# Kernel optimization log

Measured on AMD Instinct MI355X. Metric: run time of the kernel, lower is better.

The kernel has to match this reference:

```python
import jax, jax.numpy as jnp
import numpy as np

C = 128   # desc_dim
NQ = 8
NK = 32768

def setup_inputs() -> dict:
    k = jax.random.key(0)
    ks = jax.random.split(k, 9)
    query = jax.random.normal(ks[0], (1, C, NQ), dtype=jnp.float32)
    keys = jax.random.normal(ks[1], (1, C, NK), dtype=jnp.float32)
    value = jax.random.normal(ks[2], (1, C, NK), dtype=jnp.float32)
    dist = jax.random.normal(ks[3], (1, C, NQ * NK), dtype=jnp.float32)
    mask = jax.random.randint(ks[4], (1, NQ, NK), 0, 2).astype(bool)
    # MLP([3C, C, 1]) as 1x1 Conv1d weights (kernel size 1 -> plain matmuls)
    W1 = jax.random.normal(ks[5], (C, 3 * C), dtype=jnp.float32) * (1.0 / np.sqrt(3 * C))
    b1 = jax.random.normal(ks[6], (C,), dtype=jnp.float32) * 0.01
    W2 = jax.random.normal(ks[7], (1, C), dtype=jnp.float32) * (1.0 / np.sqrt(C))
    b2 = jax.random.normal(ks[8], (1,), dtype=jnp.float32) * 0.01
    return {"query": query, "keys": keys, "value": value, "dist": dist,
            "mask": mask, "W1": W1, "b1": b1, "W2": W2, "b2": b2}

def reference(query, keys, value, dist, mask, W1, b1, W2, b2):
    b = query.shape[0]
    nq, nk = query.shape[-1], keys.shape[-1]
    # pairwise concat: [b, 3C, nq*nk] (faithful to the torch repeat-expand)
    q_e = jnp.broadcast_to(query[:, :, :, None], (b, query.shape[1], nq, nk)).reshape(b, -1, nq * nk)
    k_e = jnp.broadcast_to(keys[:, :, None, :], (b, keys.shape[1], nq, nk)).reshape(b, -1, nq * nk)
    cat = jnp.concatenate([q_e, k_e, dist], axis=1)            # [b, 3C, nq*nk]
    h = jax.nn.relu(jnp.einsum('oc,bcl->bol', W1, cat) + b1[None, :, None])
    s = jnp.einsum('oc,bcl->bol', W2, h) + b2[None, :, None]   # [b, 1, nq*nk]
    scores = s.reshape(b, nq, nk)
    # mask branch (bool tensor): push masked-out entries below the min
    floor = jax.lax.stop_gradient(scores.min()) - 20.0
    scores = scores + floor * (~mask).astype(scores.dtype).reshape(1, nq, nk)
    prob = jax.nn.softmax(scores, axis=-1)                     # [b, nq, nk]
    out = jnp.einsum('bnm,bdm->bdn', prob, value)              # [b, C, nq]
    return out, scores
```

## Files before the change

kernel.cpp:

```cpp
#include <hip/hip_runtime.h>
#include <hip/hip_bf16.h>
#include <math.h>

#define C_    128
#define NQ_   8
#define NK_   32768
#define QNK_  (NQ_*NK_)
#define KW_   16
#define KTB_  64
#define NSB_  512
#define NCH_  256

#define AQ_OFF     0
#define MINKEY_OFF 1024
#define DENOM_OFF  1040
#define OUTV_OFF   4096
#define WSA_OFF    266240

typedef float f32x4 __attribute__((ext_vector_type(4)));
typedef int   i32x4 __attribute__((ext_vector_type(4)));
typedef short bf16x8 __attribute__((ext_vector_type(8)));

__device__ inline unsigned short f2bf(float f){
  unsigned u = __float_as_uint(f);
  return (unsigned short)((u + 0x7FFFu + ((u >> 16) & 1u)) >> 16);
}
__device__ inline unsigned int pkbf(float a, float b){
  __hip_bfloat162 h = __float22bfloat162_rn(make_float2(a, b));
  union { __hip_bfloat162 h2; unsigned int u; } cv; cv.h2 = h; return cv.u;
}
__device__ inline unsigned int fkey(float f){
  unsigned u = __float_as_uint(f);
  return (u & 0x80000000u) ? ~u : (u | 0x80000000u);
}
__device__ inline float fkey_dec(unsigned key){
  unsigned u = (key & 0x80000000u) ? (key & 0x7FFFFFFFu) : ~key;
  return __uint_as_float(u);
}
__device__ inline int swz8(int r){ return ((r ^ (r >> 3)) & 7) << 3; }

__global__ __launch_bounds__(256) void prep_kernel(const float* __restrict__ query,
    const float* __restrict__ W1, const float* __restrict__ b1, float* __restrict__ ws){
  const int t = threadIdx.x, b = blockIdx.x;
  if (b < 16){
    unsigned int* wsa = (unsigned int*)(ws + WSA_OFF);
    for (int u = b*1024 + t; u < (b+1)*1024; u += 256){
      unsigned int pack = 0;
#pragma unroll
      for (int e2 = 0; e2 < 2; e2++){
        const int E = u*2 + e2;
        const int f = E >> 9, lane = (E >> 3) & 63, e = E & 7;
        const int w = f >> 4, r = f & 15;
        const int part = r >> 3, ks = (r >> 1) & 3, of = r & 1;
        const int o = w*32 + of*16 + (lane & 15);
        const int c = ks*32 + ((lane >> 4) << 3) + e;
        pack |= (unsigned int)f2bf(W1[o*384 + 128 + part*128 + c]) << (16*e2);
      }
      wsa[u] = pack;
    }
  } else {
    if (t == 0) *(unsigned int*)(ws + MINKEY_OFF) = 0xFFFFFFFFu;
    if (t < 128){
      const int o = t;
      float s[8];
#pragma unroll
      for (int q = 0; q < 8; q++) s[q] = b1[o];
      for (int c = 0; c < 128; c++){
        const float wv = W1[o*384 + c];
#pragma unroll
        for (int q = 0; q < 8; q++) s[q] += wv * query[c*8 + q];
      }
#pragma unroll
      for (int q = 0; q < 8; q++) ws[AQ_OFF + q*128 + o] = s[q];
    }
  }
}

__device__ inline void stage16_load(const float* __restrict__ src, size_t rstride,
                                    int l, f32x4* ra, f32x4* rb){
  const int skl = (l & 3) * 4;
  const int c2  = (l >> 2) * 2;
#pragma unroll
  for (int p = 0; p < 4; p++){
    const float* pa = src + (size_t)(p*32 + c2)*rstride + skl;
    ra[p] = __builtin_nontemporal_load((const f32x4*)pa);
    rb[p] = __builtin_nontemporal_load((const f32x4*)(pa + rstride));
  }
}
__device__ inline void stage16_write(unsigned short* __restrict__ lds,
                                     int l, const f32x4* ra, const f32x4* rb){
  const int skl = (l & 3) * 4;
  const int c2  = (l >> 2) * 2;
#pragma unroll
  for (int p = 0; p < 4; p++){
    const int c = p*32 + c2;
#pragma unroll
    for (int j = 0; j < 4; j++){
      const int kl = skl + j;
      const int idx = (kl*128 + c) ^ swz8(kl);
      *(unsigned int*)&lds[idx] = pkbf(ra[p][j], rb[p][j]);
    }
  }
}
__device__ inline bf16x8 frag16_read(const unsigned short* __restrict__ lds,
                                     int ks, int g, int li){
  const int idx = (li << 7) + (((ks << 5) + (g << 3)) ^ swz8(li));
  return *(const bf16x8*)&lds[idx];
}

__global__ __launch_bounds__(256, 2) void scores_kernel(
    const float* __restrict__ keys, const float* __restrict__ dist,
    const float* __restrict__ W2, const float* __restrict__ b2p,
    float* __restrict__ ws, float* __restrict__ scores)
{
  __shared__ unsigned short a_lds[32*512];
  __shared__ unsigned short d_lds[4][KW_*128];
  __shared__ float aq_lds[NQ_*128];
  __shared__ float w2_lds[128];
  __shared__ float minred[4];

  const int t = threadIdx.x, w = t >> 6, l = t & 63;
  const int g = l >> 4, li = l & 15;
  const int blk = blockIdx.x;
  const int k0w = blk*KTB_ + w*KW_;
  unsigned short* dw = d_lds[w];

  const unsigned int* wsaU = (const unsigned int*)(ws + WSA_OFF);
  unsigned int* aU = (unsigned int*)a_lds;
  for (int i = t; i < 8192; i += 256){
    const int s = i >> 8, r = i & 255;
    aU[i] = wsaU[((s >> 3)*16 + (s & 7))*256 + r];
  }
  for (int i = t; i < NQ_*128; i += 256) aq_lds[i] = ws[AQ_OFF + i];
  if (t < 128) w2_lds[t] = W2[t];

  f32x4 rA[4], rB[4], rC[4], rD[4];
  stage16_load(keys + k0w, NK_, l, rA, rB);
  stage16_write(dw, l, rA, rB);
  stage16_load(dist + k0w, QNK_, l, rA, rB);
  __syncthreads();

  f32x4 bk[8];
#pragma unroll
  for (int f = 0; f < 8; f++){ f32x4 z = {0.f,0.f,0.f,0.f}; bk[f] = z; }
#pragma unroll
  for (int ks = 0; ks < 4; ks++){
    const bf16x8 bfr = frag16_read(dw, ks, g, li);
#pragma unroll
    for (int of8 = 0; of8 < 8; of8++){
      const int s = (of8 >> 1)*8 + ks*2 + (of8 & 1);
      const bf16x8 a = *(const bf16x8*)&a_lds[s*512 + l*8];
      bk[of8] = __builtin_amdgcn_mfma_f32_16x16x32_bf16(a, bfr, bk[of8], 0,0,0);
    }
  }
  __syncthreads();

  for (int i = t; i < 8192; i += 256){
    const int s = i >> 8, r = i & 255;
    aU[i] = wsaU[((s >> 3)*16 + 8 + (s & 7))*256 + r];
  }
  __syncthreads();

  const float b2v = b2p[0];
  float minv = INFINITY;

#define SCORE_ITER(Q, RA, RB, RA2, RB2)                                          \
  {                                                                              \
    if ((Q) < 7) stage16_load(dist + (size_t)((Q)+1)*NK_ + k0w, QNK_, l, RA2, RB2); \
    stage16_write(dw, l, RA, RB);                                                \
    f32x4 acc[8];                                                                \
    _Pragma("unroll")                                                            \
    for (int f = 0; f < 8; f++) acc[f] = bk[f];                                  \
    _Pragma("unroll")                                                            \
    for (int ks = 0; ks < 4; ks++){                                              \
      const bf16x8 bfr = frag16_read(dw, ks, g, li);                             \
      _Pragma("unroll")                                                          \
      for (int of8 = 0; of8 < 8; of8++){                                         \
        const int s = (of8 >> 1)*8 + ks*2 + (of8 & 1);                           \
        const bf16x8 a = *(const bf16x8*)&a_lds[s*512 + l*8];                    \
        acc[of8] = __builtin_amdgcn_mfma_f32_16x16x32_bf16(a, bfr, acc[of8], 0,0,0); \
      }                                                                          \
    }                                                                            \
    float sv = 0.f;                                                              \
    _Pragma("unroll")                                                            \
    for (int of8 = 0; of8 < 8; of8++){                                           \
      const int ob = (of8 >> 1)*32 + (of8 & 1)*16 + g*4;                         \
      const f32x4 aqv = *(const f32x4*)&aq_lds[(Q)*128 + ob];                    \
      const f32x4 w2v = *(const f32x4*)&w2_lds[ob];                              \
      _Pragma("unroll")                                                          \
      for (int r = 0; r < 4; r++)                                                \
        sv += w2v[r] * fmaxf(acc[of8][r] + aqv[r], 0.f);                         \
    }                                                                            \
    sv += __shfl_xor(sv, 16, 64);                                                \
    sv += __shfl_xor(sv, 32, 64);                                                \
    sv += b2v;                                                                   \
    if (l < 16)                                                                  \
      __builtin_nontemporal_store(sv, &scores[(size_t)(Q)*NK_ + k0w + l]);       \
    minv = fminf(minv, sv);                                                      \
  }

  SCORE_ITER(0, rA, rB, rC, rD)
  SCORE_ITER(1, rC, rD, rA, rB)
  SCORE_ITER(2, rA, rB, rC, rD)
  SCORE_ITER(3, rC, rD, rA, rB)
  SCORE_ITER(4, rA, rB, rC, rD)
  SCORE_ITER(5, rC, rD, rA, rB)
  SCORE_ITER(6, rA, rB, rC, rD)
  SCORE_ITER(7, rC, rD, rA, rB)
#undef SCORE_ITER

#pragma unroll
  for (int off = 32; off > 0; off >>= 1) minv = fminf(minv, __shfl_xor(minv, off, 64));
  if (l == 0) minred[w] = minv;
  __syncthreads();
  if (t == 0){
    const float m = fminf(fminf(minred[0], minred[1]), fminf(minred[2], minred[3]));
    atomicMin((unsigned int*)(ws + MINKEY_OFF), fkey(m));
  }
}

__global__ __launch_bounds__(256) void softmax_pv_kernel(
    const float* __restrict__ value, const int* __restrict__ mask,
    float* __restrict__ scores, float* __restrict__ ws)
{
  __shared__ float v_lds[128*128];
  __shared__ __align__(16) float e_lds[8][128];
  __shared__ float wsum[8];
  const int t = threadIdx.x, bid = blockIdx.x, k0 = bid*128;
  const float floorv = fkey_dec(*(const unsigned int*)(ws + MINKEY_OFF)) - 20.0f;

  for (int i = t; i < 4096; i += 256){
    const int d = i >> 5, k4 = (i & 31)*4;
    const f32x4 v = __builtin_nontemporal_load((const f32x4*)&value[(size_t)d*NK_ + k0 + k4]);
    const int dw = (d*128 + k4) ^ ((d & 31) << 2);
    *(f32x4*)&v_lds[dw] = v;
  }

  {
    const int q = t >> 5, kk = (t & 31)*4;
    const size_t gi = (size_t)q*NK_ + k0 + kk;
    const f32x4 s4 = *(const f32x4*)&scores[gi];
    const i32x4 m4 = *(const i32x4*)&mask[gi];
    f32x4 sf, e;
#pragma unroll
    for (int j = 0; j < 4; j++){
      sf[j] = m4[j] ? s4[j] : s4[j] + floorv;
      e[j]  = __expf(sf[j]);
    }
    __builtin_nontemporal_store(sf, (f32x4*)&scores[gi]);
    *(f32x4*)&e_lds[q][kk] = e;
    float es = e[0] + e[1] + e[2] + e[3];
#pragma unroll
    for (int off = 16; off > 0; off >>= 1) es += __shfl_xor(es, off, 64);
    if ((t & 31) == 0) wsum[q] = es;
  }
  __syncthreads();
  if (t < 8) ws[DENOM_OFF + t*NCH_ + bid] = wsum[t];

  const int d = t & 127, qb = (t >> 7)*4;
  f32x4 acc = {0.f,0.f,0.f,0.f};
#pragma unroll 8
  for (int k4 = 0; k4 < 128; k4 += 4){
    const int dw = (d*128 + k4) ^ ((d & 31) << 2);
    const f32x4 v  = *(const f32x4*)&v_lds[dw];
    const f32x4 e0 = *(const f32x4*)&e_lds[qb+0][k4];
    const f32x4 e1 = *(const f32x4*)&e_lds[qb+1][k4];
    const f32x4 e2 = *(const f32x4*)&e_lds[qb+2][k4];
    const f32x4 e3 = *(const f32x4*)&e_lds[qb+3][k4];
#pragma unroll
    for (int j = 0; j < 4; j++){
      acc[0] += v[j]*e0[j]; acc[1] += v[j]*e1[j];
      acc[2] += v[j]*e2[j]; acc[3] += v[j]*e3[j];
    }
  }
#pragma unroll
  for (int j = 0; j < 4; j++) ws[OUTV_OFF + (size_t)bid*1024 + d*8 + qb + j] = acc[j];
}

__global__ __launch_bounds__(256) void finalize_kernel(const float* __restrict__ ws,
    float* __restrict__ out){
  __shared__ float dsum[8];
  __shared__ float red[8][32];
  const int t = threadIdx.x, bid = blockIdx.x;

  if (t < 64){
    const int q = t >> 3, i = t & 7;
    float s = 0.f;
    for (int j = 0; j < 32; j++) s += ws[DENOM_OFF + q*NCH_ + i + 8*j];
#pragma unroll
    for (int off = 4; off > 0; off >>= 1) s += __shfl_xor(s, off, 64);
    if (i == 0) dsum[q] = s;
  }

  const int ol = t & 31, part = t >> 5;
  float s = 0.f;
  for (int j = 0; j < 32; j++)
    s += ws[OUTV_OFF + (size_t)(part + 8*j)*1024 + bid*32 + ol];
  red[part][ol] = s;
  __syncthreads();

  if (t < 32){
    float a = 0.f;
#pragma unroll
    for (int p = 0; p < 8; p++) a += red[p][t];
    const int o = bid*32 + t;
    out[o] = a / dsum[o & 7];
  }
}

extern "C" void kernel_launch(void* const* d_in, const int* in_sizes, int n_in,
                              void* d_out, int out_size, void* d_ws, size_t ws_size,
                              hipStream_t stream){
  const float* query=(const float*)d_in[0];
  const float* keys =(const float*)d_in[1];
  const float* value=(const float*)d_in[2];
  const float* dist =(const float*)d_in[3];
  const int*   mask =(const int*)d_in[4];
  const float* W1   =(const float*)d_in[5];
  const float* b1   =(const float*)d_in[6];
  const float* W2   =(const float*)d_in[7];
  const float* b2   =(const float*)d_in[8];
  float* out=(float*)d_out;
  float* scores=out+1024;
  float* ws=(float*)d_ws;

  prep_kernel      <<<17,256,0,stream>>>(query,W1,b1,ws);
  scores_kernel    <<<NSB_,256,0,stream>>>(keys,dist,W2,b2,ws,scores);
  softmax_pv_kernel<<<NCH_,256,0,stream>>>(value,mask,scores,ws);
  finalize_kernel  <<<32,256,0,stream>>>(ws,out);
}
```

Before: 65.69 us.

## Split scores blocks across query halves with 512-thread blocks and 128-key tiles

The scores kernel now uses 512-thread blocks covering 128 keys. Each of the 512 blocks handles one half of the query dimension, so a block runs 4 query iterations per wave instead of 8. This shortens each wave's serial chain and raises the number of resident waves, at the cost of computing the key-projection MFMA twice (once per query half) and loading the weight tile into LDS for each half. The prep kernel also splits the per-query dot product across two threads and combines them with a shuffle.

```diff
diff --git a/kernel.cpp b/kernel.cpp
--- a/kernel.cpp
+++ b/kernel.cpp
@@ -7,7 +7,7 @@
 #define NK_   32768
 #define QNK_  (NQ_*NK_)
 #define KW_   16
-#define KTB_  64
+#define KTB_  128
 #define NSB_  512
 #define NCH_  256
 
@@ -60,18 +60,19 @@
     }
   } else {
     if (t == 0) *(unsigned int*)(ws + MINKEY_OFF) = 0xFFFFFFFFu;
-    if (t < 128){
-      const int o = t;
-      float s[8];
-#pragma unroll
-      for (int q = 0; q < 8; q++) s[q] = b1[o];
-      for (int c = 0; c < 128; c++){
-        const float wv = W1[o*384 + c];
-#pragma unroll
-        for (int q = 0; q < 8; q++) s[q] += wv * query[c*8 + q];
-      }
-#pragma unroll
-      for (int q = 0; q < 8; q++) ws[AQ_OFF + q*128 + o] = s[q];
+    const int o = t >> 1, h = t & 1;
+    float s[8];
+#pragma unroll
+    for (int q = 0; q < 8; q++) s[q] = 0.f;
+    for (int c = h*64; c < h*64 + 64; c++){
+      const float wv = W1[o*384 + c];
+#pragma unroll
+      for (int q = 0; q < 8; q++) s[q] += wv * query[c*8 + q];
+    }
+#pragma unroll
+    for (int q = 0; q < 8; q++){
+      s[q] += __shfl_xor(s[q], 1, 64);
+      if (h == 0) ws[AQ_OFF + q*128 + o] = s[q] + b1[o];
     }
   }
 }
@@ -108,36 +109,37 @@
   return *(const bf16x8*)&lds[idx];
 }
 
-__global__ __launch_bounds__(256, 2) void scores_kernel(
+__global__ __launch_bounds__(512, 4) void scores_kernel(
     const float* __restrict__ keys, const float* __restrict__ dist,
     const float* __restrict__ W2, const float* __restrict__ b2p,
     float* __restrict__ ws, float* __restrict__ scores)
 {
   __shared__ unsigned short a_lds[32*512];
-  __shared__ unsigned short d_lds[4][KW_*128];
-  __shared__ float aq_lds[NQ_*128];
+  __shared__ unsigned short d_lds[8][KW_*128];
+  __shared__ float aq_lds[4*128];
   __shared__ float w2_lds[128];
-  __shared__ float minred[4];
+  __shared__ float minred[8];
 
   const int t = threadIdx.x, w = t >> 6, l = t & 63;
   const int g = l >> 4, li = l & 15;
-  const int blk = blockIdx.x;
-  const int k0w = blk*KTB_ + w*KW_;
+  const int kb = blockIdx.x >> 1, qh = blockIdx.x & 1;
+  const int q0 = qh*4;
+  const int k0w = kb*KTB_ + w*KW_;
   unsigned short* dw = d_lds[w];
 
   const unsigned int* wsaU = (const unsigned int*)(ws + WSA_OFF);
   unsigned int* aU = (unsigned int*)a_lds;
-  for (int i = t; i < 8192; i += 256){
+  for (int i = t; i < 8192; i += 512){
     const int s = i >> 8, r = i & 255;
     aU[i] = wsaU[((s >> 3)*16 + (s & 7))*256 + r];
   }
-  for (int i = t; i < NQ_*128; i += 256) aq_lds[i] = ws[AQ_OFF + i];
+  aq_lds[t & 511] = ws[AQ_OFF + q0*128 + (t & 511)];
   if (t < 128) w2_lds[t] = W2[t];
 
-  f32x4 rA[4], rB[4], rC[4], rD[4];
-  stage16_load(keys + k0w, NK_, l, rA, rB);
-  stage16_write(dw, l, rA, rB);
-  stage16_load(dist + k0w, QNK_, l, rA, rB);
+  f32x4 rA[4], rB[4], kA[4], kB[4];
+  stage16_load(keys + k0w, NK_, l, kA, kB);
+  stage16_load(dist + (size_t)q0*NK_ + k0w, QNK_, l, rA, rB);
+  stage16_write(dw, l, kA, kB);
   __syncthreads();
 
   f32x4 bk[8];
@@ -155,7 +157,7 @@
   }
   __syncthreads();
 
-  for (int i = t; i < 8192; i += 256){
+  for (int i = t; i < 8192; i += 512){
     const int s = i >> 8, r = i & 255;
     aU[i] = wsaU[((s >> 3)*16 + 8 + (s & 7))*256 + r];
   }
@@ -164,57 +166,51 @@
   const float b2v = b2p[0];
   float minv = INFINITY;
 
-#define SCORE_ITER(Q, RA, RB, RA2, RB2)                                          \
-  {                                                                              \
-    if ((Q) < 7) stage16_load(dist + (size_t)((Q)+1)*NK_ + k0w, QNK_, l, RA2, RB2); \
-    stage16_write(dw, l, RA, RB);                                                \
-    f32x4 acc[8];                                                                \
-    _Pragma("unroll")                                                            \
-    for (int f = 0; f < 8; f++) acc[f] = bk[f];                                  \
-    _Pragma("unroll")                                                            \
-    for (int ks = 0; ks < 4; ks++){                                              \
-      const bf16x8 bfr = frag16_read(dw, ks, g, li);                             \
-      _Pragma("unroll")                                                          \
-      for (int of8 = 0; of8 < 8; of8++){                                         \
-        const int s = (of8 >> 1)*8 + ks*2 + (of8 & 1);                           \
-        const bf16x8 a = *(const bf16x8*)&a_lds[s*512 + l*8];                    \
-        acc[of8] = __builtin_amdgcn_mfma_f32_16x16x32_bf16(a, bfr, acc[of8], 0,0,0); \
-      }                                                                          \
-    }                                                                            \
-    float sv = 0.f;                                                              \
-    _Pragma("unroll")                                                            \
-    for (int of8 = 0; of8 < 8; of8++){                                           \
-      const int ob = (of8 >> 1)*32 + (of8 & 1)*16 + g*4;                         \
-      const f32x4 aqv = *(const f32x4*)&aq_lds[(Q)*128 + ob];                    \
-      const f32x4 w2v = *(const f32x4*)&w2_lds[ob];                              \
-      _Pragma("unroll")                                                          \
-      for (int r = 0; r < 4; r++)                                                \
-        sv += w2v[r] * fmaxf(acc[of8][r] + aqv[r], 0.f);                         \
-    }                                                                            \
-    sv += __shfl_xor(sv, 16, 64);                                                \
-    sv += __shfl_xor(sv, 32, 64);                                                \
-    sv += b2v;                                                                   \
-    if (l < 16)                                                                  \
-      __builtin_nontemporal_store(sv, &scores[(size_t)(Q)*NK_ + k0w + l]);       \
-    minv = fminf(minv, sv);                                                      \
-  }
-
-  SCORE_ITER(0, rA, rB, rC, rD)
-  SCORE_ITER(1, rC, rD, rA, rB)
-  SCORE_ITER(2, rA, rB, rC, rD)
-  SCORE_ITER(3, rC, rD, rA, rB)
-  SCORE_ITER(4, rA, rB, rC, rD)
-  SCORE_ITER(5, rC, rD, rA, rB)
-  SCORE_ITER(6, rA, rB, rC, rD)
-  SCORE_ITER(7, rC, rD, rA, rB)
-#undef SCORE_ITER
+#pragma unroll
+  for (int qi = 0; qi < 4; qi++){
+    stage16_write(dw, l, rA, rB);
+    if (qi < 3) stage16_load(dist + (size_t)(q0+qi+1)*NK_ + k0w, QNK_, l, rA, rB);
+
+    f32x4 acc[8];
+#pragma unroll
+    for (int f = 0; f < 8; f++) acc[f] = bk[f];
+#pragma unroll
+    for (int ks = 0; ks < 4; ks++){
+      const bf16x8 bfr = frag16_read(dw, ks, g, li);
+#pragma unroll
+      for (int of8 = 0; of8 < 8; of8++){
+        const int s = (of8 >> 1)*8 + ks*2 + (of8 & 1);
+        const bf16x8 a = *(const bf16x8*)&a_lds[s*512 + l*8];
+        acc[of8] = __builtin_amdgcn_mfma_f32_16x16x32_bf16(a, bfr, acc[of8], 0,0,0);
+      }
+    }
+
+    float sv = 0.f;
+#pragma unroll
+    for (int of8 = 0; of8 < 8; of8++){
+      const int ob = (of8 >> 1)*32 + (of8 & 1)*16 + g*4;
+      const f32x4 aqv = *(const f32x4*)&aq_lds[qi*128 + ob];
+      const f32x4 w2v = *(const f32x4*)&w2_lds[ob];
+#pragma unroll
+      for (int r = 0; r < 4; r++)
+        sv += w2v[r] * fmaxf(acc[of8][r] + aqv[r], 0.f);
+    }
+    sv += __shfl_xor(sv, 16, 64);
+    sv += __shfl_xor(sv, 32, 64);
+    sv += b2v;
+    if (l < 16)
+      __builtin_nontemporal_store(sv, &scores[(size_t)(q0+qi)*NK_ + k0w + l]);
+    minv = fminf(minv, sv);
+  }
 
 #pragma unroll
   for (int off = 32; off > 0; off >>= 1) minv = fminf(minv, __shfl_xor(minv, off, 64));
   if (l == 0) minred[w] = minv;
   __syncthreads();
   if (t == 0){
-    const float m = fminf(fminf(minred[0], minred[1]), fminf(minred[2], minred[3]));
+    float m = minred[0];
+#pragma unroll
+    for (int i = 1; i < 8; i++) m = fminf(m, minred[i]);
     atomicMin((unsigned int*)(ws + MINKEY_OFF), fkey(m));
   }
 }
@@ -325,7 +321,7 @@
   float* ws=(float*)d_ws;
 
   prep_kernel      <<<17,256,0,stream>>>(query,W1,b1,ws);
-  scores_kernel    <<<NSB_,256,0,stream>>>(keys,dist,W2,b2,ws,scores);
+  scores_kernel    <<<NSB_,512,0,stream>>>(keys,dist,W2,b2,ws,scores);
   softmax_pv_kernel<<<NCH_,256,0,stream>>>(value,mask,scores,ws);
   finalize_kernel  <<<32,256,0,stream>>>(ws,out);
 }
```

Measured after the change: 85.22 us. +29.7%, slower.

## Split key projection into separate kernel and halve query work per scores block

Applied to the files above, without the earlier changes.

The per-key W1_k·keys product moves into a new bkprep kernel that stores it as bf16 in the workspace. The scores kernel then launches twice as many blocks, each covering half the queries and reading that precomputed term, with occupancy raised to 3 blocks per CU. The query-bias prep is also split across thread pairs. This aims to expose more parallelism and drop the in-kernel key GEMM and the A-fragment reload. The cost is an extra launch, workspace round-trips, and bf16 rounding of the key term.

```diff
diff --git a/kernel.cpp b/kernel.cpp
--- a/kernel.cpp
+++ b/kernel.cpp
@@ -6,9 +6,6 @@
 #define NQ_   8
 #define NK_   32768
 #define QNK_  (NQ_*NK_)
-#define KW_   16
-#define KTB_  64
-#define NSB_  512
 #define NCH_  256
 
 #define AQ_OFF     0
@@ -16,10 +13,12 @@
 #define DENOM_OFF  1040
 #define OUTV_OFF   4096
 #define WSA_OFF    266240
+#define BH_OFF     282624
 
 typedef float f32x4 __attribute__((ext_vector_type(4)));
 typedef int   i32x4 __attribute__((ext_vector_type(4)));
 typedef short bf16x8 __attribute__((ext_vector_type(8)));
+typedef unsigned int u32x2 __attribute__((ext_vector_type(2)));
 
 __device__ inline unsigned short f2bf(float f){
   unsigned u = __float_as_uint(f);
@@ -29,6 +28,8 @@
   __hip_bfloat162 h = __float22bfloat162_rn(make_float2(a, b));
   union { __hip_bfloat162 h2; unsigned int u; } cv; cv.h2 = h; return cv.u;
 }
+__device__ inline float bf_lo(unsigned u){ return __uint_as_float(u << 16); }
+__device__ inline float bf_hi(unsigned u){ return __uint_as_float(u & 0xFFFF0000u); }
 __device__ inline unsigned int fkey(float f){
   unsigned u = __float_as_uint(f);
   return (u & 0x80000000u) ? ~u : (u | 0x80000000u);
@@ -60,22 +61,24 @@
     }
   } else {
     if (t == 0) *(unsigned int*)(ws + MINKEY_OFF) = 0xFFFFFFFFu;
-    if (t < 128){
-      const int o = t;
-      float s[8];
-#pragma unroll
-      for (int q = 0; q < 8; q++) s[q] = b1[o];
-      for (int c = 0; c < 128; c++){
-        const float wv = W1[o*384 + c];
-#pragma unroll
-        for (int q = 0; q < 8; q++) s[q] += wv * query[c*8 + q];
-      }
-#pragma unroll
-      for (int q = 0; q < 8; q++) ws[AQ_OFF + q*128 + o] = s[q];
-    }
-  }
-}
-
+    const int o = t >> 1, h = t & 1;
+    float s[8];
+#pragma unroll
+    for (int q = 0; q < 8; q++) s[q] = 0.f;
+    for (int c = h*64; c < h*64 + 64; c++){
+      const float wv = W1[o*384 + c];
+#pragma unroll
+      for (int q = 0; q < 8; q++) s[q] += wv * query[c*8 + q];
+    }
+#pragma unroll
+    for (int q = 0; q < 8; q++){
+      s[q] += __shfl_xor(s[q], 1, 64);
+      if (h == 0) ws[AQ_OFF + q*128 + o] = s[q] + b1[o];
+    }
+  }
+}
+
+template<bool NT>
 __device__ inline void stage16_load(const float* __restrict__ src, size_t rstride,
                                     int l, f32x4* ra, f32x4* rb){
   const int skl = (l & 3) * 4;
@@ -83,8 +86,9 @@
 #pragma unroll
   for (int p = 0; p < 4; p++){
     const float* pa = src + (size_t)(p*32 + c2)*rstride + skl;
-    ra[p] = __builtin_nontemporal_load((const f32x4*)pa);
-    rb[p] = __builtin_nontemporal_load((const f32x4*)(pa + rstride));
+    if (NT){ ra[p] = __builtin_nontemporal_load((const f32x4*)pa);
+             rb[p] = __builtin_nontemporal_load((const f32x4*)(pa + rstride)); }
+    else   { ra[p] = *(const f32x4*)pa; rb[p] = *(const f32x4*)(pa + rstride); }
   }
 }
 __device__ inline void stage16_write(unsigned short* __restrict__ lds,
@@ -108,69 +112,99 @@
   return *(const bf16x8*)&lds[idx];
 }
 
-__global__ __launch_bounds__(256, 2) void scores_kernel(
-    const float* __restrict__ keys, const float* __restrict__ dist,
-    const float* __restrict__ W2, const float* __restrict__ b2p,
-    float* __restrict__ ws, float* __restrict__ scores)
+__global__ __launch_bounds__(256) void bkprep_kernel(const float* __restrict__ keys,
+    float* __restrict__ ws){
+  __shared__ unsigned short d_lds[4][16*128];
+  const int t = threadIdx.x, w = t >> 6, l = t & 63;
+  const int g = l >> 4, li = l & 15;
+  const int kw = blockIdx.x*4 + w;
+  const int k0w = kw*16;
+  unsigned short* dw = d_lds[w];
+
+  const bf16x8* wsa8 = (const bf16x8*)(ws + WSA_OFF);
+  bf16x8 afk[32];
+#pragma unroll
+  for (int s = 0; s < 32; s++) afk[s] = wsa8[((s >> 3)*16 + (s & 7))*64 + l];
+
+  f32x4 ra[4], rb[4];
+  stage16_load<false>(keys + k0w, NK_, l, ra, rb);
+  stage16_write(dw, l, ra, rb);
+
+  f32x4 bk[8];
+#pragma unroll
+  for (int f = 0; f < 8; f++){ f32x4 z = {0.f,0.f,0.f,0.f}; bk[f] = z; }
+#pragma unroll
+  for (int ks = 0; ks < 4; ks++){
+    const bf16x8 bfr = frag16_read(dw, ks, g, li);
+#pragma unroll
+    for (int of8 = 0; of8 < 8; of8++){
+      const int s = (of8 >> 1)*8 + ks*2 + (of8 & 1);
+      bk[of8] = __builtin_amdgcn_mfma_f32_16x16x32_bf16(afk[s], bfr, bk[of8], 0,0,0);
+    }
+  }
+
+  unsigned int* bh = (unsigned int*)(ws + BH_OFF);
+#pragma unroll
+  for (int of8 = 0; of8 < 8; of8++){
+    u32x2 p;
+    p[0] = pkbf(bk[of8][0], bk[of8][1]);
+    p[1] = pkbf(bk[of8][2], bk[of8][3]);
+    *(u32x2*)(bh + (size_t)((kw*8 + of8)*64 + l)*2) = p;
+  }
+}
+
+__global__ __launch_bounds__(256, 3) void scores_kernel(
+    const float* __restrict__ dist, const float* __restrict__ W2,
+    const float* __restrict__ b2p, float* __restrict__ ws,
+    float* __restrict__ scores)
 {
   __shared__ unsigned short a_lds[32*512];
-  __shared__ unsigned short d_lds[4][KW_*128];
-  __shared__ float aq_lds[NQ_*128];
+  __shared__ unsigned short d_lds[4][16*128];
+  __shared__ float aq_lds[4*128];
   __shared__ float w2_lds[128];
   __shared__ float minred[4];
 
   const int t = threadIdx.x, w = t >> 6, l = t & 63;
   const int g = l >> 4, li = l & 15;
-  const int blk = blockIdx.x;
-  const int k0w = blk*KTB_ + w*KW_;
+  const int kb = blockIdx.x >> 1, qh = blockIdx.x & 1;
+  const int q0 = qh*4;
+  const int kw = kb*4 + w;
+  const int k0w = kw*16;
   unsigned short* dw = d_lds[w];
 
   const unsigned int* wsaU = (const unsigned int*)(ws + WSA_OFF);
   unsigned int* aU = (unsigned int*)a_lds;
   for (int i = t; i < 8192; i += 256){
     const int s = i >> 8, r = i & 255;
-    aU[i] = wsaU[((s >> 3)*16 + (s & 7))*256 + r];
-  }
-  for (int i = t; i < NQ_*128; i += 256) aq_lds[i] = ws[AQ_OFF + i];
+    aU[i] = wsaU[((s >> 3)*16 + 8 + (s & 7))*256 + r];
+  }
+  for (int i = t; i < 512; i += 256) aq_lds[i] = ws[AQ_OFF + q0*128 + i];
   if (t < 128) w2_lds[t] = W2[t];
 
+  u32x2 bhc[8];
+  {
+    const unsigned int* bh = (const unsigned int*)(ws + BH_OFF);
+#pragma unroll
+    for (int of8 = 0; of8 < 8; of8++)
+      bhc[of8] = *(const u32x2*)(bh + (size_t)((kw*8 + of8)*64 + l)*2);
+  }
   f32x4 rA[4], rB[4], rC[4], rD[4];
-  stage16_load(keys + k0w, NK_, l, rA, rB);
-  stage16_write(dw, l, rA, rB);
-  stage16_load(dist + k0w, QNK_, l, rA, rB);
-  __syncthreads();
-
-  f32x4 bk[8];
-#pragma unroll
-  for (int f = 0; f < 8; f++){ f32x4 z = {0.f,0.f,0.f,0.f}; bk[f] = z; }
-#pragma unroll
-  for (int ks = 0; ks < 4; ks++){
-    const bf16x8 bfr = frag16_read(dw, ks, g, li);
-#pragma unroll
-    for (int of8 = 0; of8 < 8; of8++){
-      const int s = (of8 >> 1)*8 + ks*2 + (of8 & 1);
-      const bf16x8 a = *(const bf16x8*)&a_lds[s*512 + l*8];
-      bk[of8] = __builtin_amdgcn_mfma_f32_16x16x32_bf16(a, bfr, bk[of8], 0,0,0);
-    }
-  }
-  __syncthreads();
-
-  for (int i = t; i < 8192; i += 256){
-    const int s = i >> 8, r = i & 255;
-    aU[i] = wsaU[((s >> 3)*16 + 8 + (s & 7))*256 + r];
-  }
+  stage16_load<true>(dist + (size_t)q0*NK_ + k0w, QNK_, l, rA, rB);
   __syncthreads();
 
   const float b2v = b2p[0];
   float minv = INFINITY;
 
-#define SCORE_ITER(Q, RA, RB, RA2, RB2)                                          \
+#define SCORE_ITER(QI, RA, RB, RA2, RB2)                                         \
   {                                                                              \
-    if ((Q) < 7) stage16_load(dist + (size_t)((Q)+1)*NK_ + k0w, QNK_, l, RA2, RB2); \
+    if ((QI) < 3) stage16_load<true>(dist + (size_t)(q0+(QI)+1)*NK_ + k0w, QNK_, l, RA2, RB2); \
     stage16_write(dw, l, RA, RB);                                                \
     f32x4 acc[8];                                                                \
     _Pragma("unroll")                                                            \
-    for (int f = 0; f < 8; f++) acc[f] = bk[f];                                  \
+    for (int of8 = 0; of8 < 8; of8++){                                           \
+      acc[of8][0] = bf_lo(bhc[of8][0]); acc[of8][1] = bf_hi(bhc[of8][0]);        \
+      acc[of8][2] = bf_lo(bhc[of8][1]); acc[of8][3] = bf_hi(bhc[of8][1]);        \
+    }                                                                            \
     _Pragma("unroll")                                                            \
     for (int ks = 0; ks < 4; ks++){                                              \
       const bf16x8 bfr = frag16_read(dw, ks, g, li);                             \
@@ -185,7 +219,7 @@
     _Pragma("unroll")                                                            \
     for (int of8 = 0; of8 < 8; of8++){                                           \
       const int ob = (of8 >> 1)*32 + (of8 & 1)*16 + g*4;                         \
-      const f32x4 aqv = *(const f32x4*)&aq_lds[(Q)*128 + ob];                    \
+      const f32x4 aqv = *(const f32x4*)&aq_lds[(QI)*128 + ob];                   \
       const f32x4 w2v = *(const f32x4*)&w2_lds[ob];                              \
       _Pragma("unroll")                                                          \
       for (int r = 0; r < 4; r++)                                                \
@@ -195,7 +229,7 @@
     sv += __shfl_xor(sv, 32, 64);                                                \
     sv += b2v;                                                                   \
     if (l < 16)                                                                  \
-      __builtin_nontemporal_store(sv, &scores[(size_t)(Q)*NK_ + k0w + l]);       \
+      __builtin_nontemporal_store(sv, &scores[(size_t)(q0+(QI))*NK_ + k0w + l]); \
     minv = fminf(minv, sv);                                                      \
   }
 
@@ -203,10 +237,6 @@
   SCORE_ITER(1, rC, rD, rA, rB)
   SCORE_ITER(2, rA, rB, rC, rD)
   SCORE_ITER(3, rC, rD, rA, rB)
-  SCORE_ITER(4, rA, rB, rC, rD)
-  SCORE_ITER(5, rC, rD, rA, rB)
-  SCORE_ITER(6, rA, rB, rC, rD)
-  SCORE_ITER(7, rC, rD, rA, rB)
 #undef SCORE_ITER
 
 #pragma unroll
@@ -325,7 +355,8 @@
   float* ws=(float*)d_ws;
 
   prep_kernel      <<<17,256,0,stream>>>(query,W1,b1,ws);
-  scores_kernel    <<<NSB_,256,0,stream>>>(keys,dist,W2,b2,ws,scores);
+  bkprep_kernel    <<<512,256,0,stream>>>(keys,ws);
+  scores_kernel    <<<1024,256,0,stream>>>(dist,W2,b2,ws,scores);
   softmax_pv_kernel<<<NCH_,256,0,stream>>>(value,mask,scores,ws);
   finalize_kernel  <<<32,256,0,stream>>>(ws,out);
 }
```

After: 87.13 us. 1.33x slower.
